# Optimization experiments

Hardware: AMD Instinct MI355X
Metric: run time of the kernel (lower is better)

## Reference

```python
import jax, jax.numpy as jnp
import numpy as np

DECAY = 0.99
EPS = 1e-5
COMMIT_W = 1.0


def setup_inputs() -> dict:
    key = jax.random.key(0)
    k1, k2, k3 = jax.random.split(key, 3)
    N, D, K = 65536, 64, 2048
    x = jax.random.normal(k1, (N, D), dtype=jnp.float32)
    embed = jax.random.normal(k2, (K, D), dtype=jnp.float32)
    embed_avg = jax.random.normal(k3, (K, D), dtype=jnp.float32)
    cluster_size = jnp.ones((K,), dtype=jnp.float32)
    return {"x": x, "embed": embed, "embed_avg": embed_avg, "cluster_size": cluster_size}


def reference(x, embed, embed_avg, cluster_size):
    # x: [N, D], embed: [K, D]
    K = embed.shape[0]
    # squared euclidean distances [N, K] (the cdist step)
    x2 = jnp.sum(x * x, axis=-1, keepdims=True)            # [N, 1]
    e2 = jnp.sum(embed * embed, axis=-1)                    # [K]
    dist = x2 - 2.0 * (x @ embed.T) + e2[None, :]           # [N, K]
    embed_ind = jnp.argmin(dist, axis=-1)                   # [N]

    # codebook gather + straight-through estimator
    quantize = embed[embed_ind]                              # [N, D]
    commit_loss = COMMIT_W * jnp.mean((jax.lax.stop_gradient(quantize) - x) ** 2)
    quantize_st = x + jax.lax.stop_gradient(quantize - x)

    # EMA codebook update (scatter / segment-sum, no gradient)
    ones = jnp.ones(embed_ind.shape, dtype=x.dtype)
    counts = jax.ops.segment_sum(ones, embed_ind, num_segments=K)        # [K]
    embed_sum = jax.ops.segment_sum(x, embed_ind, num_segments=K)        # [K, D]
    new_cluster_size = DECAY * cluster_size + (1.0 - DECAY) * counts
    new_embed_avg = DECAY * embed_avg + (1.0 - DECAY) * embed_sum
    n = jnp.sum(new_cluster_size)
    smoothed = (new_cluster_size + EPS) / (n + K * EPS) * n              # laplace smoothing
    new_embed = new_embed_avg / smoothed[:, None]                         # [K, D]

    return quantize_st, commit_loss, embed_ind, new_embed
```

## Files before the change

### kernel.cpp

```cpp
#include <hip/hip_runtime.h>
#include <hip/hip_bf16.h>

#define N_ROWS 65536
#define DIM 64
#define KC 2048
#define NPH 32
#define DECAY_F 0.99f
#define OMD_F 0.01f
#define EPS_F 1e-5f
#define MARGIN 0.02f

typedef short  s16x8  __attribute__((ext_vector_type(8)));
typedef __bf16 bf16x8 __attribute__((ext_vector_type(8)));
typedef float  f32x4v __attribute__((ext_vector_type(4)));

__device__ __forceinline__ bf16x8 as_bf(s16x8 v) { return __builtin_bit_cast(bf16x8, v); }

static constexpr size_t WS_E2       = 0;
static constexpr size_t WS_SMOOTH   = 2048;
static constexpr size_t WS_OFFS     = 4096;
static constexpr size_t WS_ROWIDS   = 6144;
static constexpr size_t WS_EH       = 71680;
static constexpr size_t WS_EL       = 137216;
static constexpr size_t WS_COUNTS   = 202752;
static constexpr size_t WS_CURS     = 204800;
static constexpr size_t WS_LOSS     = 206848;
static constexpr size_t WS_FLAGCNT  = 206849;
static constexpr size_t WS_ESUM     = 206852;
static constexpr size_t WS_FLAGLIST = 337924;
static constexpr size_t WS_ZERO_CNT = 4098;

__device__ __forceinline__ unsigned short bf16_rne(float f) {
    unsigned u = __float_as_uint(f);
    return (unsigned short)((u + 0x7FFFu + ((u >> 16) & 1u)) >> 16);
}

__global__ __launch_bounds__(256) void vq_prep_e_kernel(
    const float* __restrict__ embed, float* __restrict__ ws) {
    const int tid = threadIdx.x;
    const int lane = tid & 63;
    const int k = blockIdx.x * 4 + (tid >> 6);

    const int gtid = blockIdx.x * 256 + tid;
    if (gtid < (int)WS_ZERO_CNT) ws[WS_COUNTS + gtid] = 0.f;

    float v = embed[(size_t)k * DIM + lane];
    float m2v = -2.f * v;
    unsigned short hb = bf16_rne(m2v);
    float hf = __uint_as_float((unsigned)hb << 16);
    unsigned short lb = bf16_rne(m2v - hf);
    ((short*)(ws + WS_EH))[(size_t)k * DIM + lane] = (short)hb;
    ((short*)(ws + WS_EL))[(size_t)k * DIM + lane] = (short)lb;

    float sq = v * v;
#pragma unroll
    for (int off = 32; off > 0; off >>= 1)
        sq += __shfl_down(sq, off, 64);
    if (lane == 0) ws[WS_E2 + k] = sq;
}

__global__ __launch_bounds__(256, 2) void vq_mfma_kernel(
    const float* __restrict__ x,
    const float* __restrict__ embed,
    float* __restrict__ ws,
    float* __restrict__ out_q,
    float* __restrict__ out_ind) {
    __shared__ __attribute__((aligned(16))) short tile_lds[2][16][512];
    __shared__ __attribute__((aligned(16))) float e2_lds[KC];

    const int tid = threadIdx.x;
    const int lane = tid & 63;
    const int wave = tid >> 6;
    const int row0 = (blockIdx.x * 4 + wave) * 32;
    const int cr = lane & 15;
    const int g = lane >> 4;

    {
        const float4* s4p = reinterpret_cast<const float4*>(ws + WS_E2);
        float4 a = s4p[tid * 2 + 0];
        float4 b = s4p[tid * 2 + 1];
        *reinterpret_cast<float4*>(&e2_lds[tid * 8 + 0]) = a;
        *reinterpret_cast<float4*>(&e2_lds[tid * 8 + 4]) = b;
    }

    s16x8 xh[2][2], xl[2][2];
#pragma unroll
    for (int f = 0; f < 2; ++f) {
#pragma unroll
        for (int kc = 0; kc < 2; ++kc) {
            const float4* p4 = reinterpret_cast<const float4*>(
                x + (size_t)(row0 + f * 16 + cr) * DIM + kc * 32 + g * 8);
            float4 u = p4[0], v = p4[1];
            s16x8 h, l;
            unsigned short hb;
            hb = bf16_rne(u.x); h[0] = (short)hb; l[0] = (short)bf16_rne(u.x - __uint_as_float((unsigned)hb << 16));
            hb = bf16_rne(u.y); h[1] = (short)hb; l[1] = (short)bf16_rne(u.y - __uint_as_float((unsigned)hb << 16));
            hb = bf16_rne(u.z); h[2] = (short)hb; l[2] = (short)bf16_rne(u.z - __uint_as_float((unsigned)hb << 16));
            hb = bf16_rne(u.w); h[3] = (short)hb; l[3] = (short)bf16_rne(u.w - __uint_as_float((unsigned)hb << 16));
            hb = bf16_rne(v.x); h[4] = (short)hb; l[4] = (short)bf16_rne(v.x - __uint_as_float((unsigned)hb << 16));
            hb = bf16_rne(v.y); h[5] = (short)hb; l[5] = (short)bf16_rne(v.y - __uint_as_float((unsigned)hb << 16));
            hb = bf16_rne(v.z); h[6] = (short)hb; l[6] = (short)bf16_rne(v.z - __uint_as_float((unsigned)hb << 16));
            hb = bf16_rne(v.w); h[7] = (short)hb; l[7] = (short)bf16_rne(v.w - __uint_as_float((unsigned)hb << 16));
            xh[f][kc] = h; xl[f][kc] = l;
        }
    }

    const short* ehp = (const short*)(ws + WS_EH);
    const short* elp = (const short*)(ws + WS_EL);

    const short* mat_base = ((wave < 2) ? ehp : elp) + (wave & 1) * 32;

#define STAGE(buf, ph)                                                                  \
    {                                                                                   \
        _Pragma("unroll")                                                               \
        for (int s4 = 0; s4 < 4; ++s4) {                                                \
            const short* gsrc = mat_base + (size_t)((ph) * 64 + s4 * 16 + cr) * DIM + g * 8; \
            __builtin_amdgcn_global_load_lds(                                           \
                (const __attribute__((address_space(1))) void*)gsrc,                    \
                (__attribute__((address_space(3))) void*)(&tile_lds[(buf)][s4 * 4 + wave][0]), \
                16, 0, 0);                                                              \
        }                                                                               \
    }

    STAGE(0, 0);
    __syncthreads();

    float b1[2] = {__builtin_inff(), __builtin_inff()};
    float b2[2] = {__builtin_inff(), __builtin_inff()};
    int   i1[2] = {0, 0};

    for (int ph = 0; ph < NPH; ++ph) {
        const int cur = ph & 1;
        if (ph + 1 < NPH) STAGE(cur ^ 1, ph + 1);

#pragma unroll
        for (int s = 0; s < 4; ++s) {
            s16x8 eh0 = *(const s16x8*)(&tile_lds[cur][s * 4 + 0][lane * 8]);
            s16x8 eh1 = *(const s16x8*)(&tile_lds[cur][s * 4 + 1][lane * 8]);
            s16x8 el0 = *(const s16x8*)(&tile_lds[cur][s * 4 + 2][lane * 8]);
            s16x8 el1 = *(const s16x8*)(&tile_lds[cur][s * 4 + 3][lane * 8]);

            const int kb = ph * 64 + s * 16 + g * 4;
            f32x4v e2v = *reinterpret_cast<const f32x4v*>(&e2_lds[kb]);

#pragma unroll
            for (int f = 0; f < 2; ++f) {
                f32x4v a = e2v;
                a = __builtin_amdgcn_mfma_f32_16x16x32_bf16(as_bf(eh0), as_bf(xh[f][0]), a, 0, 0, 0);
                a = __builtin_amdgcn_mfma_f32_16x16x32_bf16(as_bf(eh1), as_bf(xh[f][1]), a, 0, 0, 0);
                a = __builtin_amdgcn_mfma_f32_16x16x32_bf16(as_bf(el0), as_bf(xh[f][0]), a, 0, 0, 0);
                a = __builtin_amdgcn_mfma_f32_16x16x32_bf16(as_bf(el1), as_bf(xh[f][1]), a, 0, 0, 0);
                a = __builtin_amdgcn_mfma_f32_16x16x32_bf16(as_bf(eh0), as_bf(xl[f][0]), a, 0, 0, 0);
                a = __builtin_amdgcn_mfma_f32_16x16x32_bf16(as_bf(eh1), as_bf(xl[f][1]), a, 0, 0, 0);

#pragma unroll
                for (int r = 0; r < 4; ++r) {
                    float dd = a[r];
                    b2[f] = __builtin_amdgcn_fmed3f(b1[f], b2[f], dd);
                    if (dd < b1[f]) { b1[f] = dd; i1[f] = kb + r; }
                }
            }
        }
        __syncthreads();
    }
#undef STAGE

    float gap[2];
#pragma unroll
    for (int f = 0; f < 2; ++f) {
#pragma unroll
        for (int mask = 16; mask <= 32; mask <<= 1) {
            float ob1 = __shfl_xor(b1[f], mask, 64);
            int   oi1 = __shfl_xor(i1[f], mask, 64);
            float ob2 = __shfl_xor(b2[f], mask, 64);
            float nb2 = fminf(fminf(b2[f], ob2), fmaxf(b1[f], ob1));
            if (ob1 < b1[f] || (ob1 == b1[f] && oi1 < i1[f])) { b1[f] = ob1; i1[f] = oi1; }
            b2[f] = nb2;
        }
        gap[f] = b2[f] - b1[f];
        if (g == 0) {
            int row = row0 + f * 16 + cr;
            out_ind[row] = (float)i1[f];
            if (gap[f] < MARGIN) {
                int p = atomicAdd((int*)(ws + WS_FLAGCNT), 1);
                if (p >= 0 && p < N_ROWS) ((int*)(ws + WS_FLAGLIST))[p] = row;
            } else {
                atomicAdd((int*)(ws + WS_COUNTS) + i1[f], 1);
            }
        }
    }

    float lossacc = 0.f;
#pragma unroll
    for (int f = 0; f < 2; ++f) {
#pragma unroll
        for (int r = 0; r < 16; ++r) {
            int   fi_r = __shfl(i1[f], r, 64);
            float gp_r = __shfl(gap[f], r, 64);
            if (gp_r >= MARGIN) {
                int row = row0 + f * 16 + r;
                float q  = embed[(size_t)fi_r * DIM + lane];
                float xv = x[(size_t)row * DIM + lane];
                out_q[(size_t)row * DIM + lane] = q;
                float d = q - xv;
                lossacc = fmaf(d, d, lossacc);
            }
        }
    }
#pragma unroll
    for (int off = 32; off > 0; off >>= 1)
        lossacc += __shfl_down(lossacc, off, 64);
    if (lane == 0) atomicAdd(ws + WS_LOSS, lossacc);
}

__global__ __launch_bounds__(256) void vq_rescore_kernel(
    const float* __restrict__ x,
    const float* __restrict__ embed,
    float* __restrict__ ws,
    float* __restrict__ out_q,
    float* __restrict__ out_ind) {
    __shared__ float xs[DIM];
    __shared__ float bd[256];
    __shared__ int   bi[256];
    __shared__ int   smi;
    const int tid = threadIdx.x;
    int cnt = ((const int*)(ws + WS_FLAGCNT))[0];
    cnt = (cnt < 0) ? 0 : ((cnt > N_ROWS) ? N_ROWS : cnt);
    const int* flags = (const int*)(ws + WS_FLAGLIST);

    for (int f = blockIdx.x; f < cnt; f += gridDim.x) {
        const int row = flags[f] & (N_ROWS - 1);
        if (tid < DIM) xs[tid] = x[(size_t)row * DIM + tid];
        __syncthreads();
        float lb = __builtin_inff(); int li = 0;
        for (int k = tid; k < KC; k += 256) {
            const float* e = embed + (size_t)k * DIM;
            float dot = 0.f;
#pragma unroll
            for (int d = 0; d < DIM; ++d) dot = fmaf(xs[d], e[d], dot);
            float dd = ws[WS_E2 + k] - 2.f * dot;
            if (dd < lb) { lb = dd; li = k; }
        }
        bd[tid] = lb; bi[tid] = li;
        __syncthreads();
        for (int s = 128; s > 0; s >>= 1) {
            if (tid < s) {
                float ov = bd[tid + s]; int oi = bi[tid + s];
                if (ov < bd[tid] || (ov == bd[tid] && oi < bi[tid])) { bd[tid] = ov; bi[tid] = oi; }
            }
            __syncthreads();
        }
        if (tid == 0) {
            out_ind[row] = (float)bi[0];
            smi = bi[0];
            atomicAdd((int*)(ws + WS_COUNTS) + bi[0], 1);
        }
        __syncthreads();
        const int mi = smi;
        if (tid < DIM) {
            float q = embed[(size_t)mi * DIM + tid];
            float xv = xs[tid];
            out_q[(size_t)row * DIM + tid] = q;
            float d = q - xv;
            float ld = d * d;
#pragma unroll
            for (int off = 32; off > 0; off >>= 1)
                ld += __shfl_down(ld, off, 64);
            if (tid == 0) atomicAdd(ws + WS_LOSS, ld);
        }
        __syncthreads();
    }
}

__global__ __launch_bounds__(256) void vq_prefix_kernel(
    const float* __restrict__ cluster_size,
    float* __restrict__ ws,
    float* __restrict__ out_loss) {
    __shared__ int   sscan[256];
    __shared__ float sred[256];
    const int tid = threadIdx.x;
    const int* counts = (const int*)(ws + WS_COUNTS);
    int* offs = (int*)(ws + WS_OFFS);

    int lc[8];
    int tot = 0;
    float csum = 0.f;
#pragma unroll
    for (int j = 0; j < 8; ++j) {
        lc[j] = counts[tid * 8 + j];
        tot += lc[j];
        csum += cluster_size[tid * 8 + j];
    }
    sscan[tid] = tot;
    sred[tid] = csum;
    __syncthreads();
    for (int off = 1; off < 256; off <<= 1) {
        int v = (tid >= off) ? sscan[tid - off] : 0;
        __syncthreads();
        sscan[tid] += v;
        __syncthreads();
    }
    for (int s = 128; s > 0; s >>= 1) {
        if (tid < s) sred[tid] += sred[tid + s];
        __syncthreads();
    }
    int run = sscan[tid] - tot;
#pragma unroll
    for (int j = 0; j < 8; ++j) {
        offs[tid * 8 + j] = run;
        run += lc[j];
    }
    const float n = DECAY_F * sred[0] + OMD_F * (float)N_ROWS;
    const float scale = n / (n + (float)KC * EPS_F);
#pragma unroll
    for (int j = 0; j < 8; ++j) {
        int k = tid * 8 + j;
        float ncs = fmaf(OMD_F, (float)counts[k], DECAY_F * cluster_size[k]);
        ws[WS_SMOOTH + k] = (ncs + EPS_F) * scale;
    }
    if (tid == 0) out_loss[0] = ws[WS_LOSS] / (float)((size_t)N_ROWS * DIM);
}

__global__ __launch_bounds__(256) void vq_fill_kernel(
    const float* __restrict__ out_ind,
    float* __restrict__ ws) {
    const int row = blockIdx.x * blockDim.x + threadIdx.x;
    ws[WS_ESUM + row * 2 + 0] = 0.f;
    ws[WS_ESUM + row * 2 + 1] = 0.f;
    const int fi = ((int)out_ind[row]) & (KC - 1);
    const int* offs = (const int*)(ws + WS_OFFS);
    int* curs = (int*)(ws + WS_CURS);
    int* rowids = (int*)(ws + WS_ROWIDS);
    int pos = atomicAdd(&curs[fi], 1);
    int idx = offs[fi] + pos;
    if (idx >= 0 && idx < N_ROWS) rowids[idx] = row | (fi << 16);
}

__global__ __launch_bounds__(256) void vq_gather_kernel(
    const float* __restrict__ x,
    float* __restrict__ ws) {
    const int lane = threadIdx.x & 63;
    const int w = blockIdx.x * 4 + (threadIdx.x >> 6);
    const int* rowids = (const int*)(ws + WS_ROWIDS);
    float* esum = ws + WS_ESUM;

    const int e = rowids[w * 64 + lane];

    float pf[8];
#pragma unroll
    for (int j = 0; j < 8; ++j) {
        int rj = __shfl(e, j, 64) & 0xFFFF;
        pf[j] = x[(size_t)rj * DIM + lane];
    }

    float acc = 0.f;
    int kprev = (__shfl(e, 0, 64) >> 16) & (KC - 1);
#pragma unroll
    for (int i = 0; i < 64; ++i) {
        float v = pf[i & 7];
        if (i + 8 < 64) {
            int rn = __shfl(e, i + 8, 64) & 0xFFFF;
            pf[i & 7] = x[(size_t)rn * DIM + lane];
        }
        int k = (__shfl(e, i, 64) >> 16) & (KC - 1);
        if (k != kprev) {
            atomicAdd(&esum[(size_t)kprev * DIM + lane], acc);
            acc = 0.f;
            kprev = k;
        }
        acc += v;
    }
    atomicAdd(&esum[(size_t)kprev * DIM + lane], acc);
}

__global__ __launch_bounds__(256) void vq_emb_kernel(
    const float* __restrict__ embed_avg,
    const float* __restrict__ ws,
    float* __restrict__ out_embed) {
    int i = blockIdx.x * blockDim.x + threadIdx.x;
    if (i >= KC * DIM) return;
    int k = i >> 6;
    float na = fmaf(OMD_F, ws[WS_ESUM + i], DECAY_F * embed_avg[i]);
    out_embed[i] = na / ws[WS_SMOOTH + k];
}

extern "C" void kernel_launch(void* const* d_in, const int* in_sizes, int n_in,
                              void* d_out, int out_size, void* d_ws, size_t ws_size,
                              hipStream_t stream) {
    const float* x            = (const float*)d_in[0];
    const float* embed        = (const float*)d_in[1];
    const float* embed_avg    = (const float*)d_in[2];
    const float* cluster_size = (const float*)d_in[3];

    float* out      = (float*)d_out;
    float* out_q    = out;
    float* out_loss = out + (size_t)N_ROWS * DIM;
    float* out_ind  = out_loss + 1;
    float* out_emb  = out_ind + N_ROWS;

    float* ws = (float*)d_ws;

    vq_prep_e_kernel<<<KC / 4, 256, 0, stream>>>(embed, ws);
    vq_mfma_kernel<<<N_ROWS / 128, 256, 0, stream>>>(x, embed, ws, out_q, out_ind);
    vq_rescore_kernel<<<2048, 256, 0, stream>>>(x, embed, ws, out_q, out_ind);
    vq_prefix_kernel<<<1, 256, 0, stream>>>(cluster_size, ws, out_loss);
    vq_fill_kernel<<<N_ROWS / 256, 256, 0, stream>>>(out_ind, ws);
    vq_gather_kernel<<<N_ROWS / 64 / 4, 256, 0, stream>>>(x, ws);
    vq_emb_kernel<<<(KC * DIM) / 256, 256, 0, stream>>>(embed_avg, ws, out_emb);
}
```

Before: 173.0 us.

## Split codebook scan across two wave groups per block and merge via LDS

```diff
diff --git a/kernel.cpp b/kernel.cpp
--- a/kernel.cpp
+++ b/kernel.cpp
@@ -4,7 +4,7 @@
 #define N_ROWS 65536
 #define DIM 64
 #define KC 2048
-#define NPH 32
+#define NPHH 16
 #define DECAY_F 0.99f
 #define OMD_F 0.01f
 #define EPS_F 1e-5f
@@ -59,28 +59,29 @@
     if (lane == 0) ws[WS_E2 + k] = sq;
 }
 
-__global__ __launch_bounds__(256, 2) void vq_mfma_kernel(
+__global__ __launch_bounds__(512, 4) void vq_mfma_kernel(
     const float* __restrict__ x,
     const float* __restrict__ embed,
     float* __restrict__ ws,
     float* __restrict__ out_q,
     float* __restrict__ out_ind) {
-    __shared__ __attribute__((aligned(16))) short tile_lds[2][16][512];
+    __shared__ __attribute__((aligned(16))) short tile_lds[2][2][16][512];
     __shared__ __attribute__((aligned(16))) float e2_lds[KC];
+    __shared__ float mb1[128], mb2[128];
+    __shared__ int   mi1[128];
 
     const int tid = threadIdx.x;
     const int lane = tid & 63;
-    const int wave = tid >> 6;
-    const int row0 = (blockIdx.x * 4 + wave) * 32;
+    const int w = tid >> 6;
+    const int kh = w >> 2;
+    const int wq = w & 3;
+    const int row0 = blockIdx.x * 128 + wq * 32;
     const int cr = lane & 15;
     const int g = lane >> 4;
 
     {
         const float4* s4p = reinterpret_cast<const float4*>(ws + WS_E2);
-        float4 a = s4p[tid * 2 + 0];
-        float4 b = s4p[tid * 2 + 1];
-        *reinterpret_cast<float4*>(&e2_lds[tid * 8 + 0]) = a;
-        *reinterpret_cast<float4*>(&e2_lds[tid * 8 + 4]) = b;
+        *reinterpret_cast<float4*>(&e2_lds[tid * 4]) = s4p[tid];
     }
 
     s16x8 xh[2][2], xl[2][2];
@@ -108,16 +109,17 @@
     const short* ehp = (const short*)(ws + WS_EH);
     const short* elp = (const short*)(ws + WS_EL);
 
-    const short* mat_base = ((wave < 2) ? ehp : elp) + (wave & 1) * 32;
+    const short* mat_base = ((wq < 2) ? ehp : elp) + (wq & 1) * 32;
 
 #define STAGE(buf, ph)                                                                  \
     {                                                                                   \
         _Pragma("unroll")                                                               \
         for (int s4 = 0; s4 < 4; ++s4) {                                                \
-            const short* gsrc = mat_base + (size_t)((ph) * 64 + s4 * 16 + cr) * DIM + g * 8; \
+            const short* gsrc = mat_base +                                              \
+                (size_t)(((kh * NPHH + (ph)) * 64) + s4 * 16 + cr) * DIM + g * 8;       \
             __builtin_amdgcn_global_load_lds(                                           \
                 (const __attribute__((address_space(1))) void*)gsrc,                    \
-                (__attribute__((address_space(3))) void*)(&tile_lds[(buf)][s4 * 4 + wave][0]), \
+                (__attribute__((address_space(3))) void*)(&tile_lds[(buf)][kh][s4 * 4 + wq][0]), \
                 16, 0, 0);                                                              \
         }                                                                               \
     }
@@ -129,18 +131,18 @@
     float b2[2] = {__builtin_inff(), __builtin_inff()};
     int   i1[2] = {0, 0};
 
-    for (int ph = 0; ph < NPH; ++ph) {
+    for (int ph = 0; ph < NPHH; ++ph) {
         const int cur = ph & 1;
-        if (ph + 1 < NPH) STAGE(cur ^ 1, ph + 1);
+        if (ph + 1 < NPHH) STAGE(cur ^ 1, ph + 1);
 
 #pragma unroll
         for (int s = 0; s < 4; ++s) {
-            s16x8 eh0 = *(const s16x8*)(&tile_lds[cur][s * 4 + 0][lane * 8]);
-            s16x8 eh1 = *(const s16x8*)(&tile_lds[cur][s * 4 + 1][lane * 8]);
-            s16x8 el0 = *(const s16x8*)(&tile_lds[cur][s * 4 + 2][lane * 8]);
-            s16x8 el1 = *(const s16x8*)(&tile_lds[cur][s * 4 + 3][lane * 8]);
-
-            const int kb = ph * 64 + s * 16 + g * 4;
+            s16x8 eh0 = *(const s16x8*)(&tile_lds[cur][kh][s * 4 + 0][lane * 8]);
+            s16x8 eh1 = *(const s16x8*)(&tile_lds[cur][kh][s * 4 + 1][lane * 8]);
+            s16x8 el0 = *(const s16x8*)(&tile_lds[cur][kh][s * 4 + 2][lane * 8]);
+            s16x8 el1 = *(const s16x8*)(&tile_lds[cur][kh][s * 4 + 3][lane * 8]);
+
+            const int kb = (kh * NPHH + ph) * 64 + s * 16 + g * 4;
             f32x4v e2v = *reinterpret_cast<const f32x4v*>(&e2_lds[kb]);
 
 #pragma unroll
@@ -165,7 +167,6 @@
     }
 #undef STAGE
 
-    float gap[2];
 #pragma unroll
     for (int f = 0; f < 2; ++f) {
 #pragma unroll
@@ -177,6 +178,30 @@
             if (ob1 < b1[f] || (ob1 == b1[f] && oi1 < i1[f])) { b1[f] = ob1; i1[f] = oi1; }
             b2[f] = nb2;
         }
+    }
+
+    if (kh == 1 && g == 0) {
+#pragma unroll
+        for (int f = 0; f < 2; ++f) {
+            int rib = wq * 32 + f * 16 + cr;
+            mb1[rib] = b1[f];
+            mb2[rib] = b2[f];
+            mi1[rib] = i1[f];
+        }
+    }
+    __syncthreads();
+    if (kh == 1) return;
+
+    float gap[2];
+#pragma unroll
+    for (int f = 0; f < 2; ++f) {
+        int rib = wq * 32 + f * 16 + cr;
+        float ob1 = mb1[rib];
+        float ob2 = mb2[rib];
+        int   oi1 = mi1[rib];
+        float nb2 = fminf(fminf(b2[f], ob2), fmaxf(b1[f], ob1));
+        if (ob1 < b1[f]) { b1[f] = ob1; i1[f] = oi1; }
+        b2[f] = nb2;
         gap[f] = b2[f] - b1[f];
         if (g == 0) {
             int row = row0 + f * 16 + cr;
@@ -401,7 +426,7 @@
     float* ws = (float*)d_ws;
 
     vq_prep_e_kernel<<<KC / 4, 256, 0, stream>>>(embed, ws);
-    vq_mfma_kernel<<<N_ROWS / 128, 256, 0, stream>>>(x, embed, ws, out_q, out_ind);
+    vq_mfma_kernel<<<N_ROWS / 128, 512, 0, stream>>>(x, embed, ws, out_q, out_ind);
     vq_rescore_kernel<<<2048, 256, 0, stream>>>(x, embed, ws, out_q, out_ind);
     vq_prefix_kernel<<<1, 256, 0, stream>>>(cluster_size, ws, out_loss);
     vq_fill_kernel<<<N_ROWS / 256, 256, 0, stream>>>(out_ind, ws);
```

Measured after the change: 163.7 us. -5.4%, faster.
